# Kernel tuning notes

Hardware: AMD Instinct MI355X
Metric: run time of the kernel (lower is better)

The kernel has to match this reference:

```python
import jax, jax.numpy as jnp
import numpy as np

EPS = 1e-06
GEO_TEMP = 0.1
TOP_K = 32
ATTN_DIM = 256
CHANNELS = 1024
LN_EPS = 1e-05  # torch LayerNorm default


def _layernorm(x, g, b):
    mu = jnp.mean(x, axis=-1, keepdims=True)
    var = jnp.mean(jnp.square(x - mu), axis=-1, keepdims=True)
    return (x - mu) * jax.lax.rsqrt(var + LN_EPS) * g + b


def _flatten_rays(plucker):
    # plucker: [B,6,h,w] -> moments [B,N,3], dirs [B,N,3]
    b, _, h, w = plucker.shape
    rays = jnp.transpose(plucker, (0, 2, 3, 1)).reshape(b, h * w, 6)
    d = rays[..., :3]
    n = jnp.linalg.norm(d, axis=-1, keepdims=True)
    dirs = d / jnp.maximum(n, EPS)  # F.normalize semantics
    return rays[..., 3:], dirs


def _epipolar_bias(plucker_query, plucker_key):
    m_q, d_q = _flatten_rays(plucker_query)
    m_k, d_k = _flatten_rays(plucker_key)
    # reciprocal[b,i,j] = |d_q_i . m_k_j + d_k_j . m_q_i|
    reciprocal = jnp.abs(jnp.einsum('bic,bjc->bij', d_q, m_k) +
                         jnp.einsum('bjc,bic->bij', d_k, m_q))
    nq = jnp.linalg.norm(m_q, axis=-1)[:, :, None]  # [B,N,1]
    nk = jnp.linalg.norm(m_k, axis=-1)[:, None, :]  # [B,1,N]
    reciprocal = reciprocal / (nq + nk + EPS)
    geo_bias = -reciprocal / GEO_TEMP
    B, N, _ = geo_bias.shape
    if 0 < TOP_K < N:
        # keep the TOP_K smallest reciprocal entries per query row
        _, keep = jax.lax.top_k(-reciprocal, TOP_K)  # [B,N,K]
        b_idx = jnp.arange(B)[:, None, None]
        n_idx = jnp.arange(N)[None, :, None]
        drop = jnp.ones((B, N, N), dtype=bool).at[b_idx, n_idx, keep].set(False)
        geo_bias = jnp.where(drop, jnp.float32(-10000.0), geo_bias)
    return geo_bias


def setup_inputs() -> dict:
    key = jax.random.key(0)
    ks = jax.random.split(key, 12)
    B, C, h, w = 4, CHANNELS, 48, 48
    D = ATTN_DIM
    inp = {
        'query_map': jax.random.normal(ks[0], (B, C, h, w), jnp.float32),
        'key_value_map': jax.random.normal(ks[1], (B, C, h, w), jnp.float32),
        'plucker_query': jax.random.normal(ks[2], (B, 6, h, w), jnp.float32),
        'plucker_key': jax.random.normal(ks[3], (B, 6, h, w), jnp.float32),
        'ln_q_g': jnp.ones((C,), jnp.float32), 'ln_q_b': jnp.zeros((C,), jnp.float32),
        'ln_k_g': jnp.ones((C,), jnp.float32), 'ln_k_b': jnp.zeros((C,), jnp.float32),
        'Wq': jax.random.normal(ks[4], (D, C), jnp.float32) * (C ** -0.5),
        'bq': jnp.zeros((D,), jnp.float32),
        'Wk': jax.random.normal(ks[5], (D, C), jnp.float32) * (C ** -0.5),
        'bk': jnp.zeros((D,), jnp.float32),
        'Wv': jax.random.normal(ks[6], (D, C), jnp.float32) * (C ** -0.5),
        'bv': jnp.zeros((D,), jnp.float32),
        # NOTE: module zero-inits out_proj; randomized here for a non-trivial baseline
        'Wo': jax.random.normal(ks[7], (C, D), jnp.float32) * (D ** -0.5),
        'bo': jnp.zeros((C,), jnp.float32),
    }
    return inp


def reference(query_map, key_value_map, plucker_query, plucker_key,
              ln_q_g, ln_q_b, ln_k_g, ln_k_b,
              Wq, bq, Wk, bk, Wv, bv, Wo, bo):
    b, c, h, w = query_map.shape
    scale = ATTN_DIM ** (-0.5)
    # [B,C,H,W] -> [B,N,C]
    q_tokens = jnp.transpose(query_map.reshape(b, c, h * w), (0, 2, 1))
    kv_tokens = jnp.transpose(key_value_map.reshape(b, c, h * w), (0, 2, 1))
    q = _layernorm(q_tokens, ln_q_g, ln_q_b) @ Wq.T + bq
    k = _layernorm(kv_tokens, ln_k_g, ln_k_b) @ Wk.T + bk
    v = kv_tokens @ Wv.T + bv
    logits = jnp.einsum('bid,bjd->bij', q, k) * scale
    logits = logits + _epipolar_bias(plucker_query, plucker_key)
    attn = jax.nn.softmax(logits, axis=-1)
    fused = jnp.einsum('bij,bjd->bid', attn, v) @ Wo.T + bo  # [B,N,C]
    return jnp.transpose(fused, (0, 2, 1)).reshape(b, c, h, w)
```

## Files before the change

### kernel.cpp

```cpp
#include <hip/hip_runtime.h>

typedef unsigned short u16;
typedef unsigned int u32;
typedef unsigned long long u64;
typedef _Float16 f16;
typedef __attribute__((ext_vector_type(8))) _Float16 half8;
typedef __attribute__((ext_vector_type(4))) float f32x4;

#define HW 2304
#define CC 1024
#define DD 256
#define NB 4
#define CANDCAP 256
#define RANKC 33
#define GATE 0.099f
#define MAXH 512

__device__ __forceinline__ float mul_s(float a, float b) {
  float r; asm("v_mul_f32 %0, %1, %2" : "=v"(r) : "v"(a), "v"(b)); return r;
}
__device__ __forceinline__ float add_s(float a, float b) {
  float r; asm("v_add_f32 %0, %1, %2" : "=v"(r) : "v"(a), "v"(b)); return r;
}
__device__ __forceinline__ void split16(float a, u16& hi, u16& lo) {
  f16 h = (f16)a;
  float hf = (float)h;
  f16 l = (f16)(a - hf);
  __builtin_memcpy(&hi, &h, 2);
  __builtin_memcpy(&lo, &l, 2);
}

__global__ void prep_weights(const float* __restrict__ wq, const float* __restrict__ wk,
                             const float* __restrict__ wv, const float* __restrict__ wo,
                             u16* __restrict__ qh, u16* __restrict__ ql,
                             u16* __restrict__ kh, u16* __restrict__ kl,
                             u16* __restrict__ vh, u16* __restrict__ vl,
                             u16* __restrict__ oh, u16* __restrict__ ol) {
  int idx = blockIdx.x * 256 + threadIdx.x;
  for (int i = idx; i < 4 * 262144; i += 262144) {
    int which = i >> 18, loc = i & 262143;
    const float* s = (which == 0) ? wq : (which == 1) ? wk : (which == 2) ? wv : wo;
    u16* dh = (which == 0) ? qh : (which == 1) ? kh : (which == 2) ? vh : oh;
    u16* dl = (which == 0) ? ql : (which == 1) ? kl : (which == 2) ? vl : ol;
    u16 h, l; split16(s[loc], h, l);
    dh[loc] = h; dl[loc] = l;
  }
}

__global__ void prep_rays(const float* __restrict__ pq, const float* __restrict__ pk,
                          float* __restrict__ qray, float* __restrict__ kray) {
#pragma clang fp contract(off)
  int t = blockIdx.x * 256 + threadIdx.x;
  const float* src = blockIdx.y ? pk : pq;
  float* dst = blockIdx.y ? kray : qray;
  int b = t / HW, i = t % HW;
  const float* sp = src + (size_t)b * 6 * HW + i;
  float d0 = sp[0], d1 = sp[HW], d2 = sp[2 * HW];
  float m0 = sp[3 * HW], m1 = sp[4 * HW], m2 = sp[5 * HW];
  float nd = __fsqrt_rn(add_s(add_s(mul_s(d0, d0), mul_s(d1, d1)), mul_s(d2, d2)));
  float nc = fmaxf(nd, 1e-6f);
  float ix = d0 / nc, iy = d1 / nc, iz = d2 / nc;
  float nm = __fsqrt_rn(add_s(add_s(mul_s(m0, m0), mul_s(m1, m1)), mul_s(m2, m2)));
  float4* dp = (float4*)(dst + (size_t)t * 12);
  dp[0] = make_float4(m0, m1, m2, nm);
  dp[1] = make_float4(ix, iy, iz, 0.f);
  dp[2] = make_float4(d0, d1, d2, 0.f);
}

__global__ __launch_bounds__(256) void ln_stats(const float* __restrict__ qmap,
                                                const float* __restrict__ kvmap,
                                                float* __restrict__ mu_q, float* __restrict__ rs_q,
                                                float* __restrict__ mu_k, float* __restrict__ rs_k) {
  const float* src = blockIdx.z ? kvmap : qmap;
  float* mu = blockIdx.z ? mu_k : mu_q;
  float* rs = blockIdx.z ? rs_k : rs_q;
  int b = blockIdx.y;
  int i0 = blockIdx.x * 32;
  int lane = threadIdx.x & 31, strip = threadIdx.x >> 5;
  const float* p = src + (size_t)b * CC * HW + i0 + lane;
  float s = 0.f, s2 = 0.f;
  for (int c = strip; c < CC; c += 8) {
    float v = p[(size_t)c * HW];
    s += v; s2 += v * v;
  }
  __shared__ float rsum[8][32], rsq[8][32];
  rsum[strip][lane] = s; rsq[strip][lane] = s2;
  __syncthreads();
  if (threadIdx.x < 32) {
    float ts = 0.f, tq = 0.f;
    for (int k = 0; k < 8; ++k) { ts += rsum[k][lane]; tq += rsq[k][lane]; }
    float m = ts * (1.f / 1024.f);
    float var = fmaxf(tq * (1.f / 1024.f) - m * m, 0.f);
    mu[b * HW + i0 + lane] = m;
    rs[b * HW + i0 + lane] = rsqrtf(var + 1e-5f);
  }
}

__global__ __launch_bounds__(256) void proj_mfma(
    const float* __restrict__ qmap, const float* __restrict__ kvmap,
    const float* __restrict__ gq, const float* __restrict__ bgq,
    const float* __restrict__ gk, const float* __restrict__ bgk,
    const u16* __restrict__ wqh, const u16* __restrict__ wql,
    const u16* __restrict__ wkh, const u16* __restrict__ wkl,
    const u16* __restrict__ wvh, const u16* __restrict__ wvl,
    const float* __restrict__ bq, const float* __restrict__ bk, const float* __restrict__ bv,
    const float* __restrict__ muq, const float* __restrict__ rsq,
    const float* __restrict__ muk, const float* __restrict__ rsk,
    float* __restrict__ qf, float* __restrict__ kf, float* __restrict__ vf) {
  int mtile = blockIdx.x, proj = blockIdx.y, b = blockIdx.z;
  int i0 = mtile * 64;
  const float* A; const u16* Wh; const u16* Wl;
  const float* gamma; const float* beta; const float* mup; const float* rsp; const float* bias;
  float* outp;
  if (proj == 0)      { A = qmap;  Wh = wqh; Wl = wql; gamma = gq; beta = bgq; mup = muq; rsp = rsq; bias = bq; outp = qf; }
  else if (proj == 1) { A = kvmap; Wh = wkh; Wl = wkl; gamma = gk; beta = bgk; mup = muk; rsp = rsk; bias = bk; outp = kf; }
  else                { A = kvmap; Wh = wvh; Wl = wvl; gamma = nullptr; beta = nullptr; mup = nullptr; rsp = nullptr; bias = bv; outp = vf; }
  __shared__ u16 Ah[64 * 72], Al[64 * 72];
  __shared__ float mul[64], rsl[64];
  int tid = threadIdx.x;
  int lane = tid & 63, wid = tid >> 6;
  if (proj < 2 && tid < 64) {
    mul[tid] = mup[b * HW + i0 + tid];
    rsl[tid] = rsp[b * HW + i0 + tid];
  }
  __syncthreads();
  f32x4 acc[4][4] = {};
  int c_loc = tid >> 2;
  int i4 = (tid & 3) * 4;
  int rowA = lane & 15, kch = (lane >> 4) * 8;
  for (int ks = 0; ks < 16; ++ks) {
    int c0 = ks * 64;
    float gma = 1.f, bet = 0.f;
    if (proj < 2) { gma = gamma[c0 + c_loc]; bet = beta[c0 + c_loc]; }
    const float* ap = A + ((size_t)(b * CC + c0 + c_loc)) * HW + i0;
#pragma unroll
    for (int p = 0; p < 4; ++p) {
      int ib = p * 16 + i4;
      float4 v = *(const float4*)(ap + ib);
      float e0 = v.x, e1 = v.y, e2 = v.z, e3 = v.w;
      if (proj < 2) {
        e0 = (e0 - mul[ib + 0]) * rsl[ib + 0] * gma + bet;
        e1 = (e1 - mul[ib + 1]) * rsl[ib + 1] * gma + bet;
        e2 = (e2 - mul[ib + 2]) * rsl[ib + 2] * gma + bet;
        e3 = (e3 - mul[ib + 3]) * rsl[ib + 3] * gma + bet;
      }
      u16 h, l;
      split16(e0, h, l); Ah[(ib + 0) * 72 + c_loc] = h; Al[(ib + 0) * 72 + c_loc] = l;
      split16(e1, h, l); Ah[(ib + 1) * 72 + c_loc] = h; Al[(ib + 1) * 72 + c_loc] = l;
      split16(e2, h, l); Ah[(ib + 2) * 72 + c_loc] = h; Al[(ib + 2) * 72 + c_loc] = l;
      split16(e3, h, l); Ah[(ib + 3) * 72 + c_loc] = h; Al[(ib + 3) * 72 + c_loc] = l;
    }
    __syncthreads();
#pragma unroll
    for (int kk = 0; kk < 2; ++kk) {
      int ko = kk * 32 + kch;
      half8 ah[4], al[4], bh[4], bl[4];
#pragma unroll
      for (int mf = 0; mf < 4; ++mf) {
        ah[mf] = *(const half8*)&Ah[(mf * 16 + rowA) * 72 + ko];
        al[mf] = *(const half8*)&Al[(mf * 16 + rowA) * 72 + ko];
      }
#pragma unroll
      for (int nf = 0; nf < 4; ++nf) {
        size_t woff = (size_t)(wid * 64 + nf * 16 + rowA) * CC + c0 + ko;
        bh[nf] = *(const half8*)&Wh[woff];
        bl[nf] = *(const half8*)&Wl[woff];
      }
#pragma unroll
      for (int mf = 0; mf < 4; ++mf)
#pragma unroll
        for (int nf = 0; nf < 4; ++nf) {
          acc[mf][nf] = __builtin_amdgcn_mfma_f32_16x16x32_f16(ah[mf], bh[nf], acc[mf][nf], 0, 0, 0);
          acc[mf][nf] = __builtin_amdgcn_mfma_f32_16x16x32_f16(ah[mf], bl[nf], acc[mf][nf], 0, 0, 0);
          acc[mf][nf] = __builtin_amdgcn_mfma_f32_16x16x32_f16(al[mf], bh[nf], acc[mf][nf], 0, 0, 0);
        }
    }
    __syncthreads();
  }
  int r4 = (lane >> 4) * 4, cold = lane & 15;
#pragma unroll
  for (int nf = 0; nf < 4; ++nf) {
    int dcol = wid * 64 + nf * 16 + cold;
    float bsv = bias[dcol];
#pragma unroll
    for (int mf = 0; mf < 4; ++mf) {
#pragma unroll
      for (int r = 0; r < 4; ++r) {
        int irow = i0 + mf * 16 + r4 + r;
        outp[(size_t)(b * HW + irow) * DD + dcol] = acc[mf][nf][r] + bsv;
      }
    }
  }
}

__global__ void hedge_init(int* __restrict__ hcount, u32* __restrict__ gmax) {
  int t = blockIdx.x * 256 + threadIdx.x;
  if (t == 0) *hcount = 0;
  if (t < MAXH) gmax[t] = 0;
}

__global__ __launch_bounds__(64) void attn_f32(
    const float* __restrict__ qf, const float* __restrict__ kf, const float* __restrict__ vf,
    const float* __restrict__ qray, const float* __restrict__ kray,
    float* __restrict__ fusedf, float* __restrict__ dfused,
    int* __restrict__ hcount, int* __restrict__ hlist) {
#pragma clang fp contract(off)
  int flat = blockIdx.y * HW + blockIdx.x;
  int swz = (flat & 7) * ((NB * HW) / 8) + (flat >> 3);
  int b = swz / HW, i = swz - b * HW;
  int lane = threadIdx.x;
  __shared__ u32 hist[1024];
  __shared__ float qs[DD];
  __shared__ int kidx[RANKC];
  __shared__ float kr[RANKC];
  __shared__ float lgt[RANKC];
  __shared__ float wgt[RANKC];
  __shared__ float dw[RANKC];
  __shared__ int cidx[CANDCAP];
  __shared__ float cr[CANDCAP];
  __shared__ int s_alt, s_last, s_hedge;
  int tok = b * HW + i;
  ((float4*)qs)[lane] = ((const float4*)(qf + (size_t)tok * DD))[lane];
  const float* qp = qray + (size_t)tok * 12;
  float4 mq = ((const float4*)qp)[0];
  float4 dq = ((const float4*)qp)[1];
#pragma unroll
  for (int k = 0; k < 16; ++k) hist[lane * 16 + k] = 0;
  __syncthreads();
  const float* krb = kray + (size_t)b * HW * 12;
  auto rcomp = [&](int j) -> float {
    const float4* kp4 = (const float4*)(krb + (size_t)j * 12);
    float4 km = kp4[0], kd = kp4[1];
    float p0 = mul_s(dq.x, km.x), p1 = mul_s(dq.y, km.y), p2 = mul_s(dq.z, km.z);
    float s1 = add_s(add_s(p0, p2), p1);
    float q0 = mul_s(kd.x, mq.x), q1 = mul_s(kd.y, mq.y), q2 = mul_s(kd.z, mq.z);
    float s2 = add_s(add_s(q0, q2), q1);
    float num = fabsf(add_s(s1, s2));
    float den = add_s(add_s(mq.w, km.w), 1e-6f);
    return num / den;
  };
  float rreg[36];
#pragma unroll
  for (int t = 0; t < 36; ++t) {
    rreg[t] = rcomp(t * 64 + lane);
    atomicAdd(&hist[__float_as_uint(rreg[t]) >> 22], 1u);
  }
  __syncthreads();
  int own = 0;
#pragma unroll
  for (int k = 0; k < 16; ++k) own += (int)hist[lane * 16 + k];
  int incl = own;
  for (int off = 1; off < 64; off <<= 1) {
    int nn = __shfl_up(incl, off);
    if (lane >= off) incl += nn;
  }
  u64 bal = __ballot(incl >= RANKC);
  int srcl = __ffsll((long long)bal) - 1;
  int exclv = __shfl(incl - own, srcl);
  int bstar = -1, below = 0, cum = exclv;
  for (int k = 0; k < 16; ++k) {
    int cnt = (int)hist[srcl * 16 + k];
    if (bstar < 0 && cum + cnt >= RANKC) { bstar = srcl * 16 + k; below = cum; }
    cum += cnt;
  }
  int kc = 0, ccn = 0;
#pragma unroll
  for (int t = 0; t < 36; ++t) {
    int j = t * 64 + lane;
    float r = rreg[t];
    int bin = (int)(__float_as_uint(r) >> 22);
    bool isk = bin < bstar, isc = bin == bstar;
    u64 bkm = __ballot(isk);
    u64 bcm = __ballot(isc);
    u64 mymask = (1ull << lane) - 1ull;
    if (isk) { int p = kc + __popcll(bkm & mymask); kidx[p] = j; kr[p] = r; }
    if (isc) { int p = ccn + __popcll(bcm & mymask); if (p < CANDCAP) { cidx[p] = j; cr[p] = r; } }
    kc += (int)__popcll(bkm);
    ccn += (int)__popcll(bcm);
  }
  __syncthreads();
  int m = RANKC - below;
  bool usec = (ccn <= CANDCAP);
  for (int s = 0; s < m; ++s) {
    float bvv = 3.402823466e38f; int bj = 0x7fffffff; int bp = -1;
    if (usec) {
      for (int p = lane; p < ccn; p += 64) {
        float v = cr[p]; int j = cidx[p];
        if (v < bvv || (v == bvv && j < bj)) { bvv = v; bj = j; bp = p; }
      }
    } else {
      for (int t = 0; t < 36; ++t) {
        int j = t * 64 + lane;
        float v = rcomp(j);
        if ((int)(__float_as_uint(v) >> 22) != bstar) continue;
        bool used = false;
        for (int u = 0; u < s; ++u) if (kidx[below + u] == j) { used = true; break; }
        if (!used && (v < bvv || (v == bvv && j < bj))) { bvv = v; bj = j; bp = -1; }
      }
    }
#pragma unroll
    for (int off = 32; off; off >>= 1) {
      float ov = __shfl_xor(bvv, off); int oj = __shfl_xor(bj, off); int op = __shfl_xor(bp, off);
      if (ov < bvv || (ov == bvv && oj < bj)) { bvv = ov; bj = oj; bp = op; }
    }
    if (lane == 0) {
      kidx[below + s] = bj; kr[below + s] = bvv;
      if (bp >= 0) cr[bp] = 3.402823466e38f;
    }
    __syncthreads();
  }
  if (lane == 0) {
    int ia = -1, ib = -1;
    for (int t = 0; t < RANKC; ++t) {
      bool gA = (ia < 0) || (kr[t] > kr[ia]) || (kr[t] == kr[ia] && kidx[t] > kidx[ia]);
      if (gA) { ib = ia; ia = t; }
      else {
        bool gB = (ib < 0) || (kr[t] > kr[ib]) || (kr[t] == kr[ib] && kidx[t] > kidx[ib]);
        if (gB) ib = t;
      }
    }
    float tau = 0.f;
    for (int u = 0; u < 2; ++u) {
      int t = u ? ib : ia;
      const float* kp = krb + (size_t)kidx[t] * 12;
      float sp = fabsf(dq.x * kp[0]) + fabsf(dq.y * kp[1]) + fabsf(dq.z * kp[2])
               + fabsf(kp[4] * mq.x) + fabsf(kp[5] * mq.y) + fabsf(kp[6] * mq.z);
      float den = (mq.w + kp[3]) + 1e-6f;
      tau += 20.0f * 5.9604645e-08f * sp / den + 4e-7f * kr[t];
    }
    s_alt = ia; s_last = ib;
    s_hedge = ((kr[ia] - kr[ib]) < tau) ? 1 : 0;
  }
  __syncthreads();
  if (lane < RANKC) {
    const float* kp = kf + (size_t)(b * HW + kidx[lane]) * DD;
    float dot = 0.f;
#pragma unroll 8
    for (int d2 = 0; d2 < DD / 4; ++d2) {
      float4 k4 = ((const float4*)kp)[d2];
      float4 q4 = ((const float4*)qs)[d2];
      dot = fmaf(k4.x, q4.x, dot);
      dot = fmaf(k4.y, q4.y, dot);
      dot = fmaf(k4.z, q4.z, dot);
      dot = fmaf(k4.w, q4.w, dot);
    }
    lgt[lane] = dot * 0.0625f - kr[lane] / 0.1f;
  }
  __syncthreads();
  int ia = s_alt, ib = s_last, hedge = s_hedge;
  {
    float lgt_l = (lane < RANKC) ? lgt[lane] : -3.402823466e38f;
    float mv = (lane < RANKC && lane != ia) ? lgt_l : -3.402823466e38f;
#pragma unroll
    for (int off = 32; off; off >>= 1) mv = fmaxf(mv, __shfl_xor(mv, off));
    float e1 = (lane < RANKC && lane != ia) ? expf(lgt_l - mv) : 0.f;
    float z1 = e1;
#pragma unroll
    for (int off = 32; off; off >>= 1) z1 += __shfl_xor(z1, off);
    float w1 = e1 / z1;
    if (lane < RANKC) wgt[lane] = w1;
    if (hedge) {
      float mv2 = (lane < RANKC && lane != ib) ? lgt_l : -3.402823466e38f;
#pragma unroll
      for (int off = 32; off; off >>= 1) mv2 = fmaxf(mv2, __shfl_xor(mv2, off));
      float e2 = (lane < RANKC && lane != ib) ? expf(lgt_l - mv2) : 0.f;
      float z2 = e2;
#pragma unroll
      for (int off = 32; off; off >>= 1) z2 += __shfl_xor(z2, off);
      if (lane < RANKC) dw[lane] = w1 - e2 / z2;
    }
  }
  __syncthreads();
  float4 o = make_float4(0.f, 0.f, 0.f, 0.f);
  float4 od = make_float4(0.f, 0.f, 0.f, 0.f);
  const float* vb = vf + (size_t)b * HW * DD;
  for (int tt = 0; tt < RANKC; ++tt) {
    float wv = wgt[tt]; int j = kidx[tt];
    float4 vv = *(const float4*)(vb + (size_t)j * DD + lane * 4);
    o.x = fmaf(wv, vv.x, o.x);
    o.y = fmaf(wv, vv.y, o.y);
    o.z = fmaf(wv, vv.z, o.z);
    o.w = fmaf(wv, vv.w, o.w);
    if (hedge) {
      float dv = dw[tt];
      od.x = fmaf(dv, vv.x, od.x);
      od.y = fmaf(dv, vv.y, od.y);
      od.z = fmaf(dv, vv.z, od.z);
      od.w = fmaf(dv, vv.w, od.w);
    }
  }
  *(float4*)(fusedf + (size_t)tok * DD + lane * 4) = o;
  if (hedge) {
    *(float4*)(dfused + (size_t)tok * DD + lane * 4) = od;
    if (lane == 0) {
      int slot = atomicAdd(hcount, 1);
      if (slot < MAXH) hlist[slot] = tok;
    }
  }
}

__global__ __launch_bounds__(64) void hedge_norm(
    const float* __restrict__ Wo, const int* __restrict__ hcount,
    const int* __restrict__ hlist, const float* __restrict__ dfused,
    u32* __restrict__ gmax) {
  int slot = blockIdx.y;
  int cnt = *hcount; if (cnt > MAXH) cnt = MAXH;
  if (slot >= cnt) return;
  int tok = hlist[slot];
  __shared__ float dfl[DD];
  int t = threadIdx.x;
  ((float4*)dfl)[t] = ((const float4*)(dfused + (size_t)tok * DD))[t];
  __syncthreads();
  int c = blockIdx.x * 64 + t;
  const float* wr = Wo + (size_t)c * DD;
  float dot = 0.f;
#pragma unroll 8
  for (int d = 0; d < DD; d += 4) {
    float4 w4 = *(const float4*)(wr + d);
    float4 f4 = *(const float4*)(dfl + d);
    dot = fmaf(w4.x, f4.x, dot);
    dot = fmaf(w4.y, f4.y, dot);
    dot = fmaf(w4.z, f4.z, dot);
    dot = fmaf(w4.w, f4.w, dot);
  }
  float am = fabsf(dot);
#pragma unroll
  for (int off = 32; off; off >>= 1) am = fmaxf(am, __shfl_xor(am, off));
  if (t == 0) atomicMax(&gmax[slot], __float_as_uint(am));
}

__global__ __launch_bounds__(256) void hedge_apply(
    const int* __restrict__ hcount, const int* __restrict__ hlist,
    const u32* __restrict__ gmax, const float* __restrict__ dfused,
    float* __restrict__ fusedf) {
  int slot = blockIdx.x;
  int cnt = *hcount; if (cnt > MAXH) cnt = MAXH;
  if (slot >= cnt) return;
  int tok = hlist[slot];
  if (__uint_as_float(gmax[slot]) <= GATE) {
    int t = threadIdx.x;
    fusedf[(size_t)tok * DD + t] -= 0.5f * dfused[(size_t)tok * DD + t];
  }
}

__global__ __launch_bounds__(256) void out_mfma(
    const u16* __restrict__ woh, const u16* __restrict__ wol,
    const float* __restrict__ fusedf, const float* __restrict__ bo,
    float* __restrict__ out) {
  int itile = blockIdx.x, ctile = blockIdx.y, b = blockIdx.z;
  int i0 = itile * 128, c0 = ctile * 128;
  __shared__ u16 Bh[128 * 72], Bl[128 * 72];
  int tid = threadIdx.x, lane = tid & 63, wid = tid >> 6;
  int wm = (wid >> 1) * 64, wn = (wid & 1) * 64;
  f32x4 acc[4][4] = {};
  int rowA = lane & 15, kch = (lane >> 4) * 8;
  for (int ks = 0; ks < 4; ++ks) {
    int d0 = ks * 64;
#pragma unroll
    for (int p = 0; p < 4; ++p) {
      int rr = p * 32 + (tid >> 3);
      int dc = (tid & 7) * 8;
      const float* fp = &fusedf[(size_t)(b * HW + i0 + rr) * DD + d0 + dc];
      float4 f0 = *(const float4*)fp;
      float4 f1 = *(const float4*)(fp + 4);
      u16 h, l;
      split16(f0.x, h, l); Bh[rr * 72 + dc + 0] = h; Bl[rr * 72 + dc + 0] = l;
      split16(f0.y, h, l); Bh[rr * 72 + dc + 1] = h; Bl[rr * 72 + dc + 1] = l;
      split16(f0.z, h, l); Bh[rr * 72 + dc + 2] = h; Bl[rr * 72 + dc + 2] = l;
      split16(f0.w, h, l); Bh[rr * 72 + dc + 3] = h; Bl[rr * 72 + dc + 3] = l;
      split16(f1.x, h, l); Bh[rr * 72 + dc + 4] = h; Bl[rr * 72 + dc + 4] = l;
      split16(f1.y, h, l); Bh[rr * 72 + dc + 5] = h; Bl[rr * 72 + dc + 5] = l;
      split16(f1.z, h, l); Bh[rr * 72 + dc + 6] = h; Bl[rr * 72 + dc + 6] = l;
      split16(f1.w, h, l); Bh[rr * 72 + dc + 7] = h; Bl[rr * 72 + dc + 7] = l;
    }
    __syncthreads();
#pragma unroll
    for (int kk = 0; kk < 2; ++kk) {
      int ko = kk * 32 + kch;
      half8 ah[4], al[4], bh[4], bl[4];
#pragma unroll
      for (int mf = 0; mf < 4; ++mf) {
        size_t woff = (size_t)(c0 + wm + mf * 16 + rowA) * DD + d0 + ko;
        ah[mf] = *(const half8*)&woh[woff];
        al[mf] = *(const half8*)&wol[woff];
      }
#pragma unroll
      for (int nf = 0; nf < 4; ++nf) {
        bh[nf] = *(const half8*)&Bh[(wn + nf * 16 + rowA) * 72 + ko];
        bl[nf] = *(const half8*)&Bl[(wn + nf * 16 + rowA) * 72 + ko];
      }
#pragma unroll
      for (int mf = 0; mf < 4; ++mf)
#pragma unroll
        for (int nf = 0; nf < 4; ++nf) {
          acc[mf][nf] = __builtin_amdgcn_mfma_f32_16x16x32_f16(ah[mf], bh[nf], acc[mf][nf], 0, 0, 0);
          acc[mf][nf] = __builtin_amdgcn_mfma_f32_16x16x32_f16(ah[mf], bl[nf], acc[mf][nf], 0, 0, 0);
          acc[mf][nf] = __builtin_amdgcn_mfma_f32_16x16x32_f16(al[mf], bh[nf], acc[mf][nf], 0, 0, 0);
        }
    }
    __syncthreads();
  }
  int r4 = (lane >> 4) * 4, cold = lane & 15;
#pragma unroll
  for (int mf = 0; mf < 4; ++mf) {
#pragma unroll
    for (int r = 0; r < 4; ++r) {
      int crow = c0 + wm + mf * 16 + r4 + r;
      float bsv = bo[crow];
#pragma unroll
      for (int nf = 0; nf < 4; ++nf) {
        int icol = i0 + wn + nf * 16 + cold;
        out[(size_t)(b * CC + crow) * HW + icol] = acc[mf][nf][r] + bsv;
      }
    }
  }
}

extern "C" void kernel_launch(void* const* d_in, const int* in_sizes, int n_in,
                              void* d_out, int out_size, void* d_ws, size_t ws_size,
                              hipStream_t stream) {
  (void)in_sizes; (void)n_in; (void)out_size; (void)ws_size;
  const float* qmap = (const float*)d_in[0];
  const float* kvmap = (const float*)d_in[1];
  const float* pq = (const float*)d_in[2];
  const float* pk = (const float*)d_in[3];
  const float* lnqg = (const float*)d_in[4];
  const float* lnqb = (const float*)d_in[5];
  const float* lnkg = (const float*)d_in[6];
  const float* lnkb = (const float*)d_in[7];
  const float* Wq = (const float*)d_in[8];
  const float* bq = (const float*)d_in[9];
  const float* Wk = (const float*)d_in[10];
  const float* bk = (const float*)d_in[11];
  const float* Wv = (const float*)d_in[12];
  const float* bv = (const float*)d_in[13];
  const float* Wo = (const float*)d_in[14];
  const float* bo = (const float*)d_in[15];
  float* out = (float*)d_out;
  char* w = (char*)d_ws;
  size_t off = 0;
  auto take = [&](size_t n) { char* p = w + off; off += (n + 511) & ~(size_t)511; return p; };
  u16* wq_h = (u16*)take((size_t)DD * CC * 2);
  u16* wq_l = (u16*)take((size_t)DD * CC * 2);
  u16* wk_h = (u16*)take((size_t)DD * CC * 2);
  u16* wk_l = (u16*)take((size_t)DD * CC * 2);
  u16* wv_h = (u16*)take((size_t)DD * CC * 2);
  u16* wv_l = (u16*)take((size_t)DD * CC * 2);
  u16* wo_h = (u16*)take((size_t)CC * DD * 2);
  u16* wo_l = (u16*)take((size_t)CC * DD * 2);
  float* qray = (float*)take((size_t)NB * HW * 12 * 4);
  float* kray = (float*)take((size_t)NB * HW * 12 * 4);
  float* mu_q = (float*)take((size_t)NB * HW * 4);
  float* rs_q = (float*)take((size_t)NB * HW * 4);
  float* mu_k = (float*)take((size_t)NB * HW * 4);
  float* rs_k = (float*)take((size_t)NB * HW * 4);
  float* qf = (float*)take((size_t)NB * HW * DD * 4);
  float* kf = (float*)take((size_t)NB * HW * DD * 4);
  float* vf = (float*)take((size_t)NB * HW * DD * 4);
  float* fusedf = (float*)take((size_t)NB * HW * DD * 4);
  float* dfused = (float*)take((size_t)NB * HW * DD * 4);
  int* hcount = (int*)take(4);
  int* hlist = (int*)take((size_t)MAXH * 4);
  u32* gmax = (u32*)take((size_t)MAXH * 4);

  prep_weights<<<dim3(1024), 256, 0, stream>>>(Wq, Wk, Wv, Wo, wq_h, wq_l, wk_h, wk_l,
                                               wv_h, wv_l, wo_h, wo_l);
  prep_rays<<<dim3(36, 2), 256, 0, stream>>>(pq, pk, qray, kray);
  ln_stats<<<dim3(72, NB, 2), 256, 0, stream>>>(qmap, kvmap, mu_q, rs_q, mu_k, rs_k);
  hedge_init<<<dim3(2), 256, 0, stream>>>(hcount, gmax);
  proj_mfma<<<dim3(36, 3, NB), 256, 0, stream>>>(qmap, kvmap, lnqg, lnqb, lnkg, lnkb,
                                                 wq_h, wq_l, wk_h, wk_l, wv_h, wv_l,
                                                 bq, bk, bv, mu_q, rs_q, mu_k, rs_k,
                                                 qf, kf, vf);
  attn_f32<<<dim3(HW, NB), 64, 0, stream>>>(qf, kf, vf, qray, kray, fusedf, dfused,
                                            hcount, hlist);
  hedge_norm<<<dim3(16, MAXH), 64, 0, stream>>>(Wo, hcount, hlist, dfused, gmax);
  hedge_apply<<<dim3(MAXH), 256, 0, stream>>>(hcount, hlist, gmax, dfused, fusedf);
  out_mfma<<<dim3(18, 8, NB), 256, 0, stream>>>(wo_h, wo_l, fusedf, bo, out);
}
```

Measured before the change: 311.4 us.

## Pre-split fused output to fp16 hi/lo in attention and halve proj tile

The attention kernel now writes fp16 hi/lo splits of its output alongside the fp32 result, and hedge_apply keeps them updated. out_mfma then loads its B operand straight from global memory instead of converting through shared memory, which removes the LDS staging and barriers. Separately, proj_mfma's M tile shrinks from 64 to 32 rows, doubling the grid to raise occupancy and parallelism, at the cost of re-reading the weights more often. The extra split arrays add write traffic in attention, and the direct global loads in out_mfma may be less coalesced.

```diff
diff --git a/kernel.cpp b/kernel.cpp
--- a/kernel.cpp
+++ b/kernel.cpp
@@ -108,25 +108,25 @@
     const float* __restrict__ muk, const float* __restrict__ rsk,
     float* __restrict__ qf, float* __restrict__ kf, float* __restrict__ vf) {
   int mtile = blockIdx.x, proj = blockIdx.y, b = blockIdx.z;
-  int i0 = mtile * 64;
+  int i0 = mtile * 32;
   const float* A; const u16* Wh; const u16* Wl;
   const float* gamma; const float* beta; const float* mup; const float* rsp; const float* bias;
   float* outp;
   if (proj == 0)      { A = qmap;  Wh = wqh; Wl = wql; gamma = gq; beta = bgq; mup = muq; rsp = rsq; bias = bq; outp = qf; }
   else if (proj == 1) { A = kvmap; Wh = wkh; Wl = wkl; gamma = gk; beta = bgk; mup = muk; rsp = rsk; bias = bk; outp = kf; }
   else                { A = kvmap; Wh = wvh; Wl = wvl; gamma = nullptr; beta = nullptr; mup = nullptr; rsp = nullptr; bias = bv; outp = vf; }
-  __shared__ u16 Ah[64 * 72], Al[64 * 72];
-  __shared__ float mul[64], rsl[64];
+  __shared__ u16 Ah[32 * 72], Al[32 * 72];
+  __shared__ float mul[32], rsl[32];
   int tid = threadIdx.x;
   int lane = tid & 63, wid = tid >> 6;
-  if (proj < 2 && tid < 64) {
+  if (proj < 2 && tid < 32) {
     mul[tid] = mup[b * HW + i0 + tid];
     rsl[tid] = rsp[b * HW + i0 + tid];
   }
   __syncthreads();
-  f32x4 acc[4][4] = {};
+  f32x4 acc[2][4] = {};
   int c_loc = tid >> 2;
-  int i4 = (tid & 3) * 4;
+  int i8 = (tid & 3) * 8;
   int rowA = lane & 15, kch = (lane >> 4) * 8;
   for (int ks = 0; ks < 16; ++ks) {
     int c0 = ks * 64;
@@ -134,8 +134,8 @@
     if (proj < 2) { gma = gamma[c0 + c_loc]; bet = beta[c0 + c_loc]; }
     const float* ap = A + ((size_t)(b * CC + c0 + c_loc)) * HW + i0;
 #pragma unroll
-    for (int p = 0; p < 4; ++p) {
-      int ib = p * 16 + i4;
+    for (int p2 = 0; p2 < 2; ++p2) {
+      int ib = i8 + p2 * 4;
       float4 v = *(const float4*)(ap + ib);
       float e0 = v.x, e1 = v.y, e2 = v.z, e3 = v.w;
       if (proj < 2) {
@@ -154,9 +154,9 @@
 #pragma unroll
     for (int kk = 0; kk < 2; ++kk) {
       int ko = kk * 32 + kch;
-      half8 ah[4], al[4], bh[4], bl[4];
-#pragma unroll
-      for (int mf = 0; mf < 4; ++mf) {
+      half8 ah[2], al[2], bh[4], bl[4];
+#pragma unroll
+      for (int mf = 0; mf < 2; ++mf) {
         ah[mf] = *(const half8*)&Ah[(mf * 16 + rowA) * 72 + ko];
         al[mf] = *(const half8*)&Al[(mf * 16 + rowA) * 72 + ko];
       }
@@ -167,7 +167,7 @@
         bl[nf] = *(const half8*)&Wl[woff];
       }
 #pragma unroll
-      for (int mf = 0; mf < 4; ++mf)
+      for (int mf = 0; mf < 2; ++mf)
 #pragma unroll
         for (int nf = 0; nf < 4; ++nf) {
           acc[mf][nf] = __builtin_amdgcn_mfma_f32_16x16x32_f16(ah[mf], bh[nf], acc[mf][nf], 0, 0, 0);
@@ -183,7 +183,7 @@
     int dcol = wid * 64 + nf * 16 + cold;
     float bsv = bias[dcol];
 #pragma unroll
-    for (int mf = 0; mf < 4; ++mf) {
+    for (int mf = 0; mf < 2; ++mf) {
 #pragma unroll
       for (int r = 0; r < 4; ++r) {
         int irow = i0 + mf * 16 + r4 + r;
@@ -202,8 +202,8 @@
 __global__ __launch_bounds__(64) void attn_f32(
     const float* __restrict__ qf, const float* __restrict__ kf, const float* __restrict__ vf,
     const float* __restrict__ qray, const float* __restrict__ kray,
-    float* __restrict__ fusedf, float* __restrict__ dfused,
-    int* __restrict__ hcount, int* __restrict__ hlist) {
+    float* __restrict__ fusedf, u16* __restrict__ fh, u16* __restrict__ fl,
+    float* __restrict__ dfused, int* __restrict__ hcount, int* __restrict__ hlist) {
 #pragma clang fp contract(off)
   int flat = blockIdx.y * HW + blockIdx.x;
   int swz = (flat & 7) * ((NB * HW) / 8) + (flat >> 3);
@@ -390,6 +390,15 @@
     }
   }
   *(float4*)(fusedf + (size_t)tok * DD + lane * 4) = o;
+  {
+    u16 h0, l0, h1, l1, h2, l2, h3, l3;
+    split16(o.x, h0, l0); split16(o.y, h1, l1);
+    split16(o.z, h2, l2); split16(o.w, h3, l3);
+    ushort4 hv; hv.x = h0; hv.y = h1; hv.z = h2; hv.w = h3;
+    ushort4 lv; lv.x = l0; lv.y = l1; lv.z = l2; lv.w = l3;
+    *(ushort4*)(fh + (size_t)tok * DD + lane * 4) = hv;
+    *(ushort4*)(fl + (size_t)tok * DD + lane * 4) = lv;
+  }
   if (hedge) {
     *(float4*)(dfused + (size_t)tok * DD + lane * 4) = od;
     if (lane == 0) {
@@ -432,48 +441,34 @@
 __global__ __launch_bounds__(256) void hedge_apply(
     const int* __restrict__ hcount, const int* __restrict__ hlist,
     const u32* __restrict__ gmax, const float* __restrict__ dfused,
-    float* __restrict__ fusedf) {
+    float* __restrict__ fusedf, u16* __restrict__ fh, u16* __restrict__ fl) {
   int slot = blockIdx.x;
   int cnt = *hcount; if (cnt > MAXH) cnt = MAXH;
   if (slot >= cnt) return;
   int tok = hlist[slot];
   if (__uint_as_float(gmax[slot]) <= GATE) {
     int t = threadIdx.x;
-    fusedf[(size_t)tok * DD + t] -= 0.5f * dfused[(size_t)tok * DD + t];
+    size_t idx = (size_t)tok * DD + t;
+    float f = fusedf[idx] - 0.5f * dfused[idx];
+    fusedf[idx] = f;
+    u16 h, l; split16(f, h, l);
+    fh[idx] = h; fl[idx] = l;
   }
 }
 
 __global__ __launch_bounds__(256) void out_mfma(
     const u16* __restrict__ woh, const u16* __restrict__ wol,
-    const float* __restrict__ fusedf, const float* __restrict__ bo,
-    float* __restrict__ out) {
+    const u16* __restrict__ fh, const u16* __restrict__ fl,
+    const float* __restrict__ bo, float* __restrict__ out) {
   int itile = blockIdx.x, ctile = blockIdx.y, b = blockIdx.z;
   int i0 = itile * 128, c0 = ctile * 128;
-  __shared__ u16 Bh[128 * 72], Bl[128 * 72];
   int tid = threadIdx.x, lane = tid & 63, wid = tid >> 6;
   int wm = (wid >> 1) * 64, wn = (wid & 1) * 64;
   f32x4 acc[4][4] = {};
   int rowA = lane & 15, kch = (lane >> 4) * 8;
+#pragma unroll
   for (int ks = 0; ks < 4; ++ks) {
     int d0 = ks * 64;
-#pragma unroll
-    for (int p = 0; p < 4; ++p) {
-      int rr = p * 32 + (tid >> 3);
-      int dc = (tid & 7) * 8;
-      const float* fp = &fusedf[(size_t)(b * HW + i0 + rr) * DD + d0 + dc];
-      float4 f0 = *(const float4*)fp;
-      float4 f1 = *(const float4*)(fp + 4);
-      u16 h, l;
-      split16(f0.x, h, l); Bh[rr * 72 + dc + 0] = h; Bl[rr * 72 + dc + 0] = l;
-      split16(f0.y, h, l); Bh[rr * 72 + dc + 1] = h; Bl[rr * 72 + dc + 1] = l;
-      split16(f0.z, h, l); Bh[rr * 72 + dc + 2] = h; Bl[rr * 72 + dc + 2] = l;
-      split16(f0.w, h, l); Bh[rr * 72 + dc + 3] = h; Bl[rr * 72 + dc + 3] = l;
-      split16(f1.x, h, l); Bh[rr * 72 + dc + 4] = h; Bl[rr * 72 + dc + 4] = l;
-      split16(f1.y, h, l); Bh[rr * 72 + dc + 5] = h; Bl[rr * 72 + dc + 5] = l;
-      split16(f1.z, h, l); Bh[rr * 72 + dc + 6] = h; Bl[rr * 72 + dc + 6] = l;
-      split16(f1.w, h, l); Bh[rr * 72 + dc + 7] = h; Bl[rr * 72 + dc + 7] = l;
-    }
-    __syncthreads();
 #pragma unroll
     for (int kk = 0; kk < 2; ++kk) {
       int ko = kk * 32 + kch;
@@ -486,8 +481,9 @@
       }
 #pragma unroll
       for (int nf = 0; nf < 4; ++nf) {
-        bh[nf] = *(const half8*)&Bh[(wn + nf * 16 + rowA) * 72 + ko];
-        bl[nf] = *(const half8*)&Bl[(wn + nf * 16 + rowA) * 72 + ko];
+        size_t foff = (size_t)(b * HW + i0 + wn + nf * 16 + rowA) * DD + d0 + ko;
+        bh[nf] = *(const half8*)&fh[foff];
+        bl[nf] = *(const half8*)&fl[foff];
       }
 #pragma unroll
       for (int mf = 0; mf < 4; ++mf)
@@ -498,7 +494,6 @@
           acc[mf][nf] = __builtin_amdgcn_mfma_f32_16x16x32_f16(al[mf], bh[nf], acc[mf][nf], 0, 0, 0);
         }
     }
-    __syncthreads();
   }
   int r4 = (lane >> 4) * 4, cold = lane & 15;
 #pragma unroll
@@ -558,6 +553,8 @@
   float* kf = (float*)take((size_t)NB * HW * DD * 4);
   float* vf = (float*)take((size_t)NB * HW * DD * 4);
   float* fusedf = (float*)take((size_t)NB * HW * DD * 4);
+  u16* fh = (u16*)take((size_t)NB * HW * DD * 2);
+  u16* fl = (u16*)take((size_t)NB * HW * DD * 2);
   float* dfused = (float*)take((size_t)NB * HW * DD * 4);
   int* hcount = (int*)take(4);
   int* hlist = (int*)take((size_t)MAXH * 4);
@@ -568,13 +565,13 @@
   prep_rays<<<dim3(36, 2), 256, 0, stream>>>(pq, pk, qray, kray);
   ln_stats<<<dim3(72, NB, 2), 256, 0, stream>>>(qmap, kvmap, mu_q, rs_q, mu_k, rs_k);
   hedge_init<<<dim3(2), 256, 0, stream>>>(hcount, gmax);
-  proj_mfma<<<dim3(36, 3, NB), 256, 0, stream>>>(qmap, kvmap, lnqg, lnqb, lnkg, lnkb,
+  proj_mfma<<<dim3(72, 3, NB), 256, 0, stream>>>(qmap, kvmap, lnqg, lnqb, lnkg, lnkb,
                                                  wq_h, wq_l, wk_h, wk_l, wv_h, wv_l,
                                                  bq, bk, bv, mu_q, rs_q, mu_k, rs_k,
                                                  qf, kf, vf);
-  attn_f32<<<dim3(HW, NB), 64, 0, stream>>>(qf, kf, vf, qray, kray, fusedf, dfused,
-                                            hcount, hlist);
+  attn_f32<<<dim3(HW, NB), 64, 0, stream>>>(qf, kf, vf, qray, kray, fusedf, fh, fl,
+                                            dfused, hcount, hlist);
   hedge_norm<<<dim3(16, MAXH), 64, 0, stream>>>(Wo, hcount, hlist, dfused, gmax);
-  hedge_apply<<<dim3(MAXH), 256, 0, stream>>>(hcount, hlist, gmax, dfused, fusedf);
-  out_mfma<<<dim3(18, 8, NB), 256, 0, stream>>>(wo_h, wo_l, fusedf, bo, out);
-}
+  hedge_apply<<<dim3(MAXH), 256, 0, stream>>>(hcount, hlist, gmax, dfused, fusedf, fh, fl);
+  out_mfma<<<dim3(18, 8, NB), 256, 0, stream>>>(wo_h, wo_l, fh, fl, bo, out);
+}
```

Result: slower. 365.5 us (+17.4%).
